# Performance work log

Measured on AMD Instinct MI355X. Metric: run time of the kernel, lower is better.

The kernel has to match this reference:

```python
import jax, jax.numpy as jnp
import numpy as np

N_GENES = 2000
D_MODEL = 256
N_LAYERS = 4
D_STATE = 16
D_CONV = 4
EXPAND = 2
D_INNER = EXPAND * D_MODEL  # 512
DT_RANK = (D_MODEL + 15) // 16  # 16


def layer_norm(x, w, b, eps=1e-5):
    mu = jnp.mean(x, axis=-1, keepdims=True)
    var = jnp.mean((x - mu) ** 2, axis=-1, keepdims=True)
    return (x - mu) * jax.lax.rsqrt(var + eps) * w + b


def mamba_mixer(h, in_w, cw, cb, xp_w, dtp_w, dtp_b, A_log, Dvec, out_w):
    # h: [B, L, d_model]
    B, L, _ = h.shape
    xz = jnp.einsum('bld,ed->ble', h, in_w)            # [B,L,2*Di]
    u, z = jnp.split(xz, 2, axis=-1)                    # [B,L,Di] each
    # causal depthwise conv1d (kernel D_CONV)
    up = jnp.pad(u, ((0, 0), (D_CONV - 1, 0), (0, 0)))
    u = sum(up[:, k:k + L, :] * cw[:, k] for k in range(D_CONV)) + cb
    u = jax.nn.silu(u)
    # input-dependent dt, B, C
    xdbc = jnp.einsum('bld,ed->ble', u, xp_w)           # [B,L,dt_rank+2N]
    dt_r = xdbc[..., :DT_RANK]
    Bm = xdbc[..., DT_RANK:DT_RANK + D_STATE]           # [B,L,N]
    Cm = xdbc[..., DT_RANK + D_STATE:]                  # [B,L,N]
    dt = jax.nn.softplus(jnp.einsum('blr,dr->bld', dt_r, dtp_w) + dtp_b)  # [B,L,Di]
    A = -jnp.exp(A_log)                                 # [Di,N]
    dA = jnp.exp(dt[..., None] * A)                     # [B,L,Di,N]
    dBu = dt[..., None] * Bm[:, :, None, :] * u[..., None]

    def step(hst, inp):
        a, bu = inp
        hst = a * hst + bu
        return hst, hst

    h0 = jnp.zeros((B, D_INNER, D_STATE), dA.dtype)
    _, hs = jax.lax.scan(step, h0, (jnp.moveaxis(dA, 1, 0), jnp.moveaxis(dBu, 1, 0)))
    y = jnp.einsum('lbdn,lbn->bld', hs, jnp.moveaxis(Cm, 1, 0)) + u * Dvec
    y = y * jax.nn.silu(z)
    return jnp.einsum('bld,ed->ble', y, out_w)          # [B,L,d_model]


def setup_inputs() -> dict:
    key = jax.random.key(0)
    ks = jax.random.split(key, 16)
    nl = N_LAYERS
    inp = {
        'x': jax.random.normal(ks[0], (2, N_GENES), jnp.float32),
        'bulk_in_w': jax.random.normal(ks[1], (D_MODEL,), jnp.float32),
        'bulk_in_b': jnp.zeros((D_MODEL,), jnp.float32),
        'gene_emb': jax.random.normal(ks[2], (1, N_GENES, D_MODEL), jnp.float32) * 0.02,
        'mod_emb': jax.random.normal(ks[3], (1, 1, D_MODEL), jnp.float32) * 0.02,
        'ln_w': jnp.ones((nl, D_MODEL), jnp.float32),
        'ln_b': jnp.zeros((nl, D_MODEL), jnp.float32),
        'in_proj_w': jax.random.normal(ks[4], (nl, 2 * D_INNER, D_MODEL), jnp.float32) * (D_MODEL ** -0.5),
        'conv_w': jax.random.normal(ks[5], (nl, D_INNER, D_CONV), jnp.float32) * (D_CONV ** -0.5),
        'conv_b': jnp.zeros((nl, D_INNER), jnp.float32),
        'x_proj_w': jax.random.normal(ks[6], (nl, DT_RANK + 2 * D_STATE, D_INNER), jnp.float32) * (D_INNER ** -0.5),
        'dt_proj_w': jax.random.normal(ks[7], (nl, D_INNER, DT_RANK), jnp.float32) * 0.01,
        'dt_proj_b': jnp.full((nl, D_INNER), -4.0, jnp.float32),
        'A_log': jnp.broadcast_to(jnp.log(jnp.arange(1, D_STATE + 1, dtype=jnp.float32)), (nl, D_INNER, D_STATE)).copy(),
        'D': jnp.ones((nl, D_INNER), jnp.float32),
        'out_proj_w': jax.random.normal(ks[8], (nl, D_MODEL, D_INNER), jnp.float32) * (D_INNER ** -0.5),
        'fin_w': jnp.ones((D_MODEL,), jnp.float32),
        'fin_b': jnp.zeros((D_MODEL,), jnp.float32),
        'head_w': jax.random.normal(ks[9], (D_MODEL,), jnp.float32) * (D_MODEL ** -0.5),
        'head_b': jnp.zeros((), jnp.float32),
    }
    return inp


def reference(x, bulk_in_w, bulk_in_b, gene_emb, mod_emb, ln_w, ln_b, in_proj_w,
              conv_w, conv_b, x_proj_w, dt_proj_w, dt_proj_b, A_log, D, out_proj_w,
              fin_w, fin_b, head_w, head_b):
    # token embed (modality='bulk'); Linear(1,d_model) == x[...,None]*w + b
    h = x[..., None] * bulk_in_w + bulk_in_b + gene_emb + mod_emb  # [B,L,d_model]
    for i in range(N_LAYERS):
        h = h + mamba_mixer(layer_norm(h, ln_w[i], ln_b[i]), in_proj_w[i], conv_w[i],
                            conv_b[i], x_proj_w[i], dt_proj_w[i], dt_proj_b[i],
                            A_log[i], D[i], out_proj_w[i])
    h = layer_norm(h, fin_w, fin_b)
    y = jnp.einsum('bld,d->bl', h, head_w) + head_b  # bulk head, squeeze(-1)
    return y
```

## Files before the change

### kernel.cpp

```cpp
#include <hip/hip_runtime.h>
#include <math.h>

#define B_  2
#define L_  2000
#define DM_ 256
#define DI_ 512
#define DS_ 16
#define NL_ 4
#define BL_ (B_*L_)
#define BLP_ 4096
#define NC_ 125
#define CL_ 16
#define NST_ (B_*DI_*DS_)

typedef unsigned short ushort_t;
typedef __attribute__((ext_vector_type(8))) short bf16x8;
typedef __attribute__((ext_vector_type(4))) float f32x4;

__device__ __forceinline__ float siluf(float x) {
    return x / (1.f + __expf(-x));
}

__device__ __forceinline__ ushort_t f2bf(float x) {
    unsigned int u = __float_as_uint(x);
    unsigned int r = (u + 0x7FFFu + ((u >> 16) & 1u)) >> 16;
    return (ushort_t)r;
}

__device__ __forceinline__ float bf2f(ushort_t v) {
    return __uint_as_float(((unsigned int)v) << 16);
}

__global__ __launch_bounds__(256) void embed_f2bf_kernel(
    const float* __restrict__ x, const float* __restrict__ biw,
    const float* __restrict__ bib, const float* __restrict__ ge,
    const float* __restrict__ me, float* __restrict__ h,
    float2* __restrict__ stats,
    const float* __restrict__ s0, const float* __restrict__ s1,
    const float* __restrict__ s2, ushort_t* __restrict__ d0,
    ushort_t* __restrict__ d1, ushort_t* __restrict__ d2,
    int N0, int N1, int N2)
{
    if (blockIdx.x < BL_) {
        __shared__ float sm[8];
        int bl = blockIdx.x, d = threadIdx.x;
        int l = bl % L_;
        float v = x[bl]*biw[d] + bib[d] + ge[(size_t)l*DM_ + d] + me[d];
        h[(size_t)bl*DM_ + d] = v;
        float s = v, q = v*v;
        #pragma unroll
        for (int o = 32; o > 0; o >>= 1) {
            s += __shfl_down(s, o);
            q += __shfl_down(q, o);
        }
        if ((d & 63) == 0) { sm[d >> 6] = s; sm[4 + (d >> 6)] = q; }
        __syncthreads();
        if (d == 0) {
            stats[bl] = make_float2(sm[0]+sm[1]+sm[2]+sm[3], sm[4]+sm[5]+sm[6]+sm[7]);
            stats[BLP_ + bl]   = make_float2(0.f, 0.f);
            stats[2*BLP_ + bl] = make_float2(0.f, 0.f);
            stats[3*BLP_ + bl] = make_float2(0.f, 0.f);
        }
    } else {
        int i = (blockIdx.x - BL_)*256 + threadIdx.x;
        const float* s; ushort_t* d; int j;
        if (i < N0)           { s = s0; d = d0; j = i; }
        else if (i < N0+N1)   { s = s1; d = d1; j = i - N0; }
        else if (i < N0+N1+N2){ s = s2; d = d2; j = i - N0 - N1; }
        else return;
        float4 v = *(const float4*)(s + 4*j);
        ushort_t o[4] = {f2bf(v.x), f2bf(v.y), f2bf(v.z), f2bf(v.w)};
        *(ushort2*)(d + 4*j)     = *(ushort2*)&o[0];
        *(ushort2*)(d + 4*j + 2) = *(ushort2*)&o[2];
    }
}

__global__ __launch_bounds__(256) void gemm_ln_mfma(
    const float* __restrict__ H, const float2* __restrict__ stats,
    const float* __restrict__ lnw, const float* __restrict__ lnb,
    const ushort_t* __restrict__ W, ushort_t* __restrict__ C, int ldc)
{
    __shared__ ushort_t a_s[128*64];
    __shared__ ushort_t b_s[128*64];
    const int r0 = blockIdx.x*128, c0 = blockIdx.y*128;
    const int tid = threadIdx.x;
    const int lane = tid & 63, w = tid >> 6;
    const int wm = (w & 1)*64, wn = (w >> 1)*64;
    const int qd = lane >> 4, l16 = lane & 15;
    f32x4 acc[4][4] = {};
    for (int kc = 0; kc < DM_; kc += 64) {
        #pragma unroll
        for (int q = 0; q < 4; q++) {
            int ch = tid + 256*q;
            int row = ch >> 3, col8 = (ch & 7)*8;
            int grow = r0 + row;
            float2 t0 = stats[grow], t1 = stats[BLP_ + grow];
            float2 t2 = stats[2*BLP_ + grow], t3 = stats[3*BLP_ + grow];
            float sum = t0.x + t1.x + t2.x + t3.x;
            float ssq = t0.y + t1.y + t2.y + t3.y;
            float mu  = sum * (1.f/DM_);
            float inv = rsqrtf(fmaxf(ssq*(1.f/DM_) - mu*mu, 0.f) + 1e-5f);
            const float* hp = H + (size_t)grow*DM_ + kc + col8;
            float4 h0 = *(const float4*)hp, h1 = *(const float4*)(hp + 4);
            const float* wp = lnw + kc + col8;
            const float* bp = lnb + kc + col8;
            float4 w0 = *(const float4*)wp, w1 = *(const float4*)(wp + 4);
            float4 b0 = *(const float4*)bp, b1 = *(const float4*)(bp + 4);
            __align__(16) ushort_t o[8];
            o[0] = f2bf((h0.x - mu)*inv*w0.x + b0.x);
            o[1] = f2bf((h0.y - mu)*inv*w0.y + b0.y);
            o[2] = f2bf((h0.z - mu)*inv*w0.z + b0.z);
            o[3] = f2bf((h0.w - mu)*inv*w0.w + b0.w);
            o[4] = f2bf((h1.x - mu)*inv*w1.x + b1.x);
            o[5] = f2bf((h1.y - mu)*inv*w1.y + b1.y);
            o[6] = f2bf((h1.z - mu)*inv*w1.z + b1.z);
            o[7] = f2bf((h1.w - mu)*inv*w1.w + b1.w);
            *(uint4*)&a_s[row*64 + col8] = *(const uint4*)o;
            *(bf16x8*)&b_s[row*64 + col8] =
                *(const bf16x8*)(W + (size_t)(c0 + row)*DM_ + kc + col8);
        }
        __syncthreads();
        #pragma unroll
        for (int ks = 0; ks < 2; ks++) {
            bf16x8 af[4], bf[4];
            #pragma unroll
            for (int i = 0; i < 4; i++)
                af[i] = *(const bf16x8*)&a_s[(wm + i*16 + l16)*64 + ks*32 + qd*8];
            #pragma unroll
            for (int j = 0; j < 4; j++)
                bf[j] = *(const bf16x8*)&b_s[(wn + j*16 + l16)*64 + ks*32 + qd*8];
            #pragma unroll
            for (int i = 0; i < 4; i++) {
                #pragma unroll
                for (int j = 0; j < 4; j++)
                    acc[i][j] = __builtin_amdgcn_mfma_f32_16x16x32_bf16(
                        af[i], bf[j], acc[i][j], 0, 0, 0);
            }
        }
        __syncthreads();
    }
    #pragma unroll
    for (int i = 0; i < 4; i++) {
        #pragma unroll
        for (int j = 0; j < 4; j++) {
            #pragma unroll
            for (int r = 0; r < 4; r++) {
                int row = r0 + wm + i*16 + qd*4 + r;
                int col = c0 + wn + j*16 + l16;
                C[(size_t)row*ldc + col] = f2bf(acc[i][j][r]);
            }
        }
    }
}

__global__ __launch_bounds__(256) void conv_xproj_kernel(
    const ushort_t* __restrict__ xz, const float* __restrict__ cw,
    const float* __restrict__ cb, const ushort_t* __restrict__ XWb,
    const float* __restrict__ DTW, const float* __restrict__ DTB,
    const float* __restrict__ Alog,
    ushort_t* __restrict__ u_bf, float* __restrict__ bn,
    float* __restrict__ cn, ushort_t* __restrict__ dtn,
    float2* __restrict__ sa)
{
    __shared__ ushort_t xs[19][520];
    __shared__ ushort_t us[16][520];
    __shared__ float ps[4*16*48];
    __shared__ float dtr_s[16][16];
    const int c = blockIdx.x, b = blockIdx.y;
    const int l0 = c * 16;
    const int tid = threadIdx.x;
    const int lane = tid & 63, w = tid >> 6;
    const int qd = lane >> 4, l16 = lane & 15;
    for (int f = tid; f < 19*64; f += 256) {
        int row = f >> 6, c8 = (f & 63)*8;
        int l = l0 - 3 + row;
        uint4 v = {0u, 0u, 0u, 0u};
        if (l >= 0)
            v = *(const uint4*)(xz + (size_t)(b*L_ + l)*1024 + c8);
        *(uint4*)&xs[row][c8] = v;
    }
    __syncthreads();
    #pragma unroll
    for (int q = 0; q < 2; q++) {
        int ch = tid + q*256;
        float4 wv = *(const float4*)(cw + ch*4);
        float bias = cb[ch];
        float x0 = bf2f(xs[0][ch]);
        float x1 = bf2f(xs[1][ch]);
        float x2 = bf2f(xs[2][ch]);
        #pragma unroll
        for (int j = 0; j < 16; j++) {
            float x3 = bf2f(xs[3 + j][ch]);
            float v = fmaf(x0, wv.x, fmaf(x1, wv.y, fmaf(x2, wv.z, fmaf(x3, wv.w, bias))));
            us[j][ch] = f2bf(siluf(v));
            x0 = x1; x1 = x2; x2 = x3;
        }
    }
    __syncthreads();
    for (int f = tid; f < 16*64; f += 256) {
        int row = f >> 6, c8 = (f & 63)*8;
        *(uint4*)(u_bf + (size_t)(b*L_ + l0 + row)*512 + c8) =
            *(const uint4*)&us[row][c8];
    }
    f32x4 acc[3] = {};
    #pragma unroll
    for (int step = 0; step < 4; step++) {
        int k = w*128 + step*32 + qd*8;
        bf16x8 af = *(const bf16x8*)&us[l16][k];
        #pragma unroll
        for (int j = 0; j < 3; j++) {
            bf16x8 bf = *(const bf16x8*)(XWb + (size_t)(j*16 + l16)*512 + k);
            acc[j] = __builtin_amdgcn_mfma_f32_16x16x32_bf16(af, bf, acc[j], 0, 0, 0);
        }
    }
    #pragma unroll
    for (int j = 0; j < 3; j++) {
        #pragma unroll
        for (int r = 0; r < 4; r++)
            ps[(w*16 + qd*4 + r)*48 + j*16 + l16] = acc[j][r];
    }
    __syncthreads();
    #pragma unroll
    for (int e = tid; e < 768; e += 256)
        ps[e] = ps[e] + ps[768 + e] + ps[1536 + e] + ps[2304 + e];
    __syncthreads();
    {
        int row = tid >> 4, n = tid & 15;
        dtr_s[row][n] = ps[row*48 + n];
        size_t base = ((size_t)(b*L_) + l0 + row)*DS_ + n;
        bn[base] = ps[row*48 + 16 + n];
        cn[base] = ps[row*48 + 32 + n];
    }
    __syncthreads();
    #pragma unroll
    for (int q = 0; q < 2; q++) {
        int d = tid + q*256;
        float wreg[16];
        const float4* wp = (const float4*)(DTW + (size_t)d*16);
        #pragma unroll
        for (int k4 = 0; k4 < 4; k4++) {
            float4 v = wp[k4];
            wreg[4*k4+0] = v.x; wreg[4*k4+1] = v.y;
            wreg[4*k4+2] = v.z; wreg[4*k4+3] = v.w;
        }
        float bias = DTB[d];
        float dtv[16];
        #pragma unroll
        for (int r = 0; r < 16; r++) {
            float a = bias;
            #pragma unroll
            for (int k = 0; k < 16; k++) a = fmaf(dtr_s[r][k], wreg[k], a);
            float dt = a > 20.f ? a : log1pf(__expf(a));
            ushort_t dtb16 = f2bf(dt);
            dtn[((size_t)(b*L_) + l0 + r)*DI_ + d] = dtb16;
            dtv[r] = bf2f(dtb16);
        }
        float Ac[DS_], s[DS_], ap[DS_];
        const float* ar = Alog + (size_t)d*DS_;
        #pragma unroll
        for (int n = 0; n < DS_; n++) { Ac[n] = -__expf(ar[n]); s[n] = 0.f; ap[n] = 1.f; }
        #pragma unroll
        for (int l = 0; l < 16; l++) {
            float dt = dtv[l];
            float u  = bf2f(us[l][d]);
            float dtu = dt*u;
            #pragma unroll
            for (int n = 0; n < DS_; n++) {
                float e = __expf(dt*Ac[n]);
                s[n] = fmaf(e, s[n], dtu*ps[l*48 + 16 + n]);
                ap[n] *= e;
            }
        }
        size_t ib = (((size_t)c*B_ + b)*DI_ + d)*DS_;
        float2* sap = sa + ib;
        #pragma unroll
        for (int k = 0; k < 8; k++) {
            float4 t = make_float4(s[2*k], ap[2*k], s[2*k+1], ap[2*k+1]);
            *(float4*)&sap[2*k] = t;
        }
    }
}

__global__ __launch_bounds__(64) void scan_phase2(
    const float2* __restrict__ sa, float* __restrict__ sinc)
{
    const int t = blockIdx.x*64 + threadIdx.x;
    float s = 0.f;
    for (int g = 0; g < 5; g++) {
        float2 v[25];
        #pragma unroll
        for (int i = 0; i < 25; i++)
            v[i] = sa[(size_t)(g*25 + i)*NST_ + t];
        #pragma unroll
        for (int i = 0; i < 25; i++) {
            sinc[(size_t)(g*25 + i)*NST_ + t] = s;
            s = fmaf(v[i].y, s, v[i].x);
        }
    }
}

template<int LAST>
__global__ __launch_bounds__(512) void phase3_fused(
    const ushort_t* __restrict__ dtn, const ushort_t* __restrict__ u_bf,
    const float* __restrict__ bn, const float* __restrict__ cn,
    const float* __restrict__ Alog, const float* __restrict__ Dv,
    const float* __restrict__ sinc, const ushort_t* __restrict__ xz,
    const ushort_t* __restrict__ opw, float* __restrict__ h,
    const float* __restrict__ lnw, const float* __restrict__ lnb,
    const ushort_t* __restrict__ ipw, ushort_t* __restrict__ xz_out,
    const float* __restrict__ hw, const float* __restrict__ hb,
    float* __restrict__ out)
{
    __shared__ float b_sh[CL_*DS_];
    __shared__ float c_sh[CL_*DS_];
    __shared__ ushort_t ys[16][520];
    __shared__ ushort_t a_sh[16][264];
    __shared__ float2 red2[8*16];
    __shared__ float2 muv[16];
    const int c = blockIdx.x, b = blockIdx.y;
    const int l0 = c*CL_;
    const int tid = threadIdx.x;
    const int w = tid >> 6, lane = tid & 63;
    const int qd = lane >> 4, l16 = lane & 15;
    {
        int f = tid & 255;
        size_t src = ((size_t)(b*L_) + l0)*DS_ + f;
        if (tid < 256) b_sh[f] = bn[src];
        else           c_sh[f] = cn[src];
    }
    const int d = tid;
    float Ac[DS_], s[DS_];
    {
        const float* ar = Alog + (size_t)d*DS_;
        #pragma unroll
        for (int n = 0; n < DS_; n++) Ac[n] = -__expf(ar[n]);
        size_t base = (((size_t)c*B_ + b)*DI_ + d)*DS_;
        #pragma unroll
        for (int n4 = 0; n4 < 4; n4++)
            *(float4*)&s[4*n4] = *(const float4*)(sinc + base + 4*n4);
    }
    const float Dd = Dv[d];
    __syncthreads();
    const ushort_t* dtp = dtn  + ((size_t)(b*L_ + l0))*DI_ + d;
    const ushort_t* up  = u_bf + ((size_t)(b*L_ + l0))*DI_ + d;
    const ushort_t* zp  = xz   + ((size_t)(b*L_ + l0))*1024 + 512 + d;
    for (int l = 0; l < CL_; l++) {
        float dt = bf2f(dtp[(size_t)l*DI_]);
        float u  = bf2f(up[(size_t)l*DI_]);
        float z  = bf2f(zp[(size_t)l*1024]);
        float dtu = dt*u;
        float y = u*Dd;
        #pragma unroll
        for (int n = 0; n < DS_; n++) {
            float e = __expf(dt*Ac[n]);
            s[n] = fmaf(e, s[n], dtu*b_sh[l*DS_ + n]);
            y = fmaf(s[n], c_sh[l*DS_ + n], y);
        }
        ys[l][d] = f2bf(y * siluf(z));
    }
    __syncthreads();
    f32x4 acc[2] = {};
    #pragma unroll
    for (int ks = 0; ks < 16; ks++) {
        bf16x8 af = *(const bf16x8*)&ys[l16][ks*32 + qd*8];
        #pragma unroll
        for (int j = 0; j < 2; j++) {
            bf16x8 bfv = *(const bf16x8*)(opw + (size_t)(w*32 + j*16 + l16)*DI_ + ks*32 + qd*8);
            acc[j] = __builtin_amdgcn_mfma_f32_16x16x32_bf16(af, bfv, acc[j], 0, 0, 0);
        }
    }
    float v[2][4];
    #pragma unroll
    for (int r = 0; r < 4; r++) {
        int lrow = qd*4 + r;
        size_t gr = (size_t)(b*L_ + l0 + lrow);
        float sm = 0.f, sq = 0.f;
        #pragma unroll
        for (int j = 0; j < 2; j++) {
            int col = w*32 + j*16 + l16;
            size_t idx = gr*DM_ + col;
            float vv = h[idx] + acc[j][r];
            if (!LAST) h[idx] = vv;
            v[j][r] = vv;
            sm += vv; sq += vv*vv;
        }
        sm += __shfl_xor(sm, 1); sq += __shfl_xor(sq, 1);
        sm += __shfl_xor(sm, 2); sq += __shfl_xor(sq, 2);
        sm += __shfl_xor(sm, 4); sq += __shfl_xor(sq, 4);
        sm += __shfl_xor(sm, 8); sq += __shfl_xor(sq, 8);
        if (l16 == 0) red2[w*16 + lrow] = make_float2(sm, sq);
    }
    __syncthreads();
    if (tid < 16) {
        float sm = 0.f, sq = 0.f;
        #pragma unroll
        for (int ww = 0; ww < 8; ww++) {
            float2 t = red2[ww*16 + tid];
            sm += t.x; sq += t.y;
        }
        float mu  = sm*(1.f/DM_);
        float inv = rsqrtf(fmaxf(sq*(1.f/DM_) - mu*mu, 0.f) + 1e-5f);
        muv[tid] = make_float2(mu, inv);
    }
    __syncthreads();
    if (!LAST) {
        #pragma unroll
        for (int r = 0; r < 4; r++) {
            int lrow = qd*4 + r;
            float2 mi = muv[lrow];
            #pragma unroll
            for (int j = 0; j < 2; j++) {
                int col = w*32 + j*16 + l16;
                a_sh[lrow][col] = f2bf((v[j][r] - mi.x)*mi.y*lnw[col] + lnb[col]);
            }
        }
        __syncthreads();
        f32x4 acc2[8] = {};
        const int n0 = w*128;
        #pragma unroll
        for (int ks = 0; ks < 8; ks++) {
            bf16x8 af = *(const bf16x8*)&a_sh[l16][ks*32 + qd*8];
            #pragma unroll
            for (int j2 = 0; j2 < 8; j2++) {
                bf16x8 bfv = *(const bf16x8*)(ipw + (size_t)(n0 + j2*16 + l16)*DM_ + ks*32 + qd*8);
                acc2[j2] = __builtin_amdgcn_mfma_f32_16x16x32_bf16(af, bfv, acc2[j2], 0, 0, 0);
            }
        }
        #pragma unroll
        for (int j2 = 0; j2 < 8; j2++) {
            #pragma unroll
            for (int r = 0; r < 4; r++) {
                size_t row = (size_t)(b*L_ + l0 + qd*4 + r);
                xz_out[row*1024 + n0 + j2*16 + l16] = f2bf(acc2[j2][r]);
            }
        }
    } else {
        float hd[4];
        #pragma unroll
        for (int r = 0; r < 4; r++) {
            int lrow = qd*4 + r;
            float2 mi = muv[lrow];
            float a = 0.f;
            #pragma unroll
            for (int j = 0; j < 2; j++) {
                int col = w*32 + j*16 + l16;
                float nv = (v[j][r] - mi.x)*mi.y*lnw[col] + lnb[col];
                a = fmaf(nv, hw[col], a);
            }
            hd[r] = a;
        }
        #pragma unroll
        for (int r = 0; r < 4; r++) {
            float x = hd[r];
            x += __shfl_xor(x, 1); x += __shfl_xor(x, 2);
            x += __shfl_xor(x, 4); x += __shfl_xor(x, 8);
            if (l16 == 0) red2[w*16 + qd*4 + r].x = x;
        }
        __syncthreads();
        if (tid < 16) {
            float x = 0.f;
            #pragma unroll
            for (int ww = 0; ww < 8; ww++) x += red2[ww*16 + tid].x;
            out[(size_t)(b*L_) + l0 + tid] = x + hb[0];
        }
    }
}

extern "C" void kernel_launch(void* const* d_in, const int* in_sizes, int n_in,
                              void* d_out, int out_size, void* d_ws, size_t ws_size,
                              hipStream_t stream)
{
    const float* x    = (const float*)d_in[0];
    const float* biw  = (const float*)d_in[1];
    const float* bib  = (const float*)d_in[2];
    const float* ge   = (const float*)d_in[3];
    const float* me   = (const float*)d_in[4];
    const float* lnw  = (const float*)d_in[5];
    const float* lnb  = (const float*)d_in[6];
    const float* ipw  = (const float*)d_in[7];
    const float* cw   = (const float*)d_in[8];
    const float* cb   = (const float*)d_in[9];
    const float* xpw  = (const float*)d_in[10];
    const float* dtw  = (const float*)d_in[11];
    const float* dtb  = (const float*)d_in[12];
    const float* alog = (const float*)d_in[13];
    const float* Dv   = (const float*)d_in[14];
    const float* opw  = (const float*)d_in[15];
    const float* fw   = (const float*)d_in[16];
    const float* fb   = (const float*)d_in[17];
    const float* hw   = (const float*)d_in[18];
    const float* hb   = (const float*)d_in[19];
    float* out = (float*)d_out;

    float* ws  = (float*)d_ws;
    float* h      = ws;
    float2* stats = (float2*)(h + (size_t)BLP_*DM_);
    float* bn     = (float*)(stats + 4*BLP_);
    float* cn     = bn + (size_t)B_*L_*DS_;
    float2* sa    = (float2*)(cn + (size_t)B_*L_*DS_);
    float* sinc   = (float*)(sa + (size_t)NC_*NST_);
    ushort_t* xz_bf = (ushort_t*)(sinc + (size_t)NC_*NST_);
    ushort_t* u_bf  = xz_bf + (size_t)BLP_*1024;
    ushort_t* dtn   = u_bf + (size_t)BLP_*DI_;
    ushort_t* ipwb  = dtn + (size_t)B_*L_*DI_;
    ushort_t* opwb  = ipwb + (size_t)NL_*1024*DM_;
    ushort_t* xpwb  = opwb + (size_t)NL_*DM_*DI_;

    const int N0 = NL_*1024*DM_/4, N1 = NL_*DM_*DI_/4, N2 = NL_*48*512/4;
    const int conv_blocks = (N0+N1+N2 + 255)/256;
    embed_f2bf_kernel<<<BL_ + conv_blocks, 256, 0, stream>>>(
        x, biw, bib, ge, me, h, stats,
        ipw, opw, xpw, ipwb, opwb, xpwb, N0, N1, N2);

    gemm_ln_mfma<<<dim3(BLP_/128, 1024/128), 256, 0, stream>>>(
        h, stats, lnw, lnb, ipwb, xz_bf, 1024);

    for (int i = 0; i < NL_; i++) {
        conv_xproj_kernel<<<dim3(NC_, B_), 256, 0, stream>>>(
            xz_bf, cw + i*DI_*4, cb + i*DI_, xpwb + (size_t)i*48*512,
            dtw + (size_t)i*DI_*16, dtb + i*DI_, alog + (size_t)i*DI_*DS_,
            u_bf, bn, cn, dtn, sa);
        scan_phase2<<<NST_/64, 64, 0, stream>>>(sa, sinc);
        if (i < NL_-1) {
            phase3_fused<0><<<dim3(NC_, B_), 512, 0, stream>>>(
                dtn, u_bf, bn, cn, alog + (size_t)i*DI_*DS_, Dv + i*DI_,
                sinc, xz_bf, opwb + (size_t)i*DM_*DI_, h,
                lnw + (i+1)*DM_, lnb + (i+1)*DM_,
                ipwb + (size_t)(i+1)*1024*DM_, xz_bf,
                nullptr, nullptr, nullptr);
        } else {
            phase3_fused<1><<<dim3(NC_, B_), 512, 0, stream>>>(
                dtn, u_bf, bn, cn, alog + (size_t)i*DI_*DS_, Dv + i*DI_,
                sinc, xz_bf, opwb + (size_t)i*DM_*DI_, h,
                fw, fb,
                nullptr, xz_bf,
                hw, hb, out);
        }
    }
}
```

Measured before the change: 414.3 us.

## Fuse all stages into one persistent cooperative kernel with grid syncs

```diff
diff --git a/kernel.cpp b/kernel.cpp
--- a/kernel.cpp
+++ b/kernel.cpp
@@ -1,468 +1,446 @@
 #include <hip/hip_runtime.h>
+#include <hip/hip_cooperative_groups.h>
 #include <math.h>
 
-#define B_  2
-#define L_  2000
-#define DM_ 256
-#define DI_ 512
-#define DS_ 16
-#define NL_ 4
-#define BL_ (B_*L_)
+namespace cg = cooperative_groups;
+
+#define B_   2
+#define L_   2000
+#define DM_  256
+#define DI_  512
+#define DS_  16
+#define NL_  4
+#define BL_  (B_*L_)
 #define BLP_ 4096
-#define NC_ 125
-#define CL_ 16
+#define NC_  125
+#define CL_  16
 #define NST_ (B_*DI_*DS_)
+#define NBLK_ 256
+#define NTHR_ 512
 
 typedef unsigned short ushort_t;
 typedef __attribute__((ext_vector_type(8))) short bf16x8;
 typedef __attribute__((ext_vector_type(4))) float f32x4;
 
-__device__ __forceinline__ float siluf(float x) {
-    return x / (1.f + __expf(-x));
-}
-
+__device__ __forceinline__ float siluf(float x) { return x / (1.f + __expf(-x)); }
 __device__ __forceinline__ ushort_t f2bf(float x) {
     unsigned int u = __float_as_uint(x);
-    unsigned int r = (u + 0x7FFFu + ((u >> 16) & 1u)) >> 16;
-    return (ushort_t)r;
+    return (ushort_t)((u + 0x7FFFu + ((u >> 16) & 1u)) >> 16);
 }
-
 __device__ __forceinline__ float bf2f(ushort_t v) {
     return __uint_as_float(((unsigned int)v) << 16);
 }
 
-__global__ __launch_bounds__(256) void embed_f2bf_kernel(
-    const float* __restrict__ x, const float* __restrict__ biw,
-    const float* __restrict__ bib, const float* __restrict__ ge,
-    const float* __restrict__ me, float* __restrict__ h,
-    float2* __restrict__ stats,
-    const float* __restrict__ s0, const float* __restrict__ s1,
-    const float* __restrict__ s2, ushort_t* __restrict__ d0,
-    ushort_t* __restrict__ d1, ushort_t* __restrict__ d2,
-    int N0, int N1, int N2)
+union SharedU {
+    struct { float sm[2][8]; } e;
+    struct { ushort_t a_s[128*64]; ushort_t b_s[128*64]; } g;
+    struct { ushort_t xs[19][520]; ushort_t us[16][520];
+             float ps[8*16*48]; float dtr[16][16]; } c;
+    struct { float b_sh[CL_*DS_]; float c_sh[CL_*DS_];
+             ushort_t ys[16][520]; ushort_t a_sh[16][264];
+             float2 red2[8*16]; float2 muv[16]; } p;
+};
+
+struct KP {
+    const float *x,*biw,*bib,*ge,*me,*lnw,*lnb,*ipw,*cw,*cb,*xpw,*dtw,*dtb,*alog,*Dv,*opw,*fw,*fb,*hw,*hb;
+    float *out;
+    float *h; float2 *stats; float *bn,*cn; float2 *sa; float *sinc;
+    ushort_t *xz,*u_bf,*dtn,*ipwb,*opwb,*xpwb;
+    int N0,N1,N2;
+};
+
+__global__ __launch_bounds__(NTHR_, 2) void mega(KP p)
 {
-    if (blockIdx.x < BL_) {
-        __shared__ float sm[8];
-        int bl = blockIdx.x, d = threadIdx.x;
-        int l = bl % L_;
-        float v = x[bl]*biw[d] + bib[d] + ge[(size_t)l*DM_ + d] + me[d];
-        h[(size_t)bl*DM_ + d] = v;
-        float s = v, q = v*v;
-        #pragma unroll
-        for (int o = 32; o > 0; o >>= 1) {
-            s += __shfl_down(s, o);
-            q += __shfl_down(q, o);
-        }
-        if ((d & 63) == 0) { sm[d >> 6] = s; sm[4 + (d >> 6)] = q; }
-        __syncthreads();
-        if (d == 0) {
-            stats[bl] = make_float2(sm[0]+sm[1]+sm[2]+sm[3], sm[4]+sm[5]+sm[6]+sm[7]);
-            stats[BLP_ + bl]   = make_float2(0.f, 0.f);
-            stats[2*BLP_ + bl] = make_float2(0.f, 0.f);
-            stats[3*BLP_ + bl] = make_float2(0.f, 0.f);
-        }
-    } else {
-        int i = (blockIdx.x - BL_)*256 + threadIdx.x;
-        const float* s; ushort_t* d; int j;
-        if (i < N0)           { s = s0; d = d0; j = i; }
-        else if (i < N0+N1)   { s = s1; d = d1; j = i - N0; }
-        else if (i < N0+N1+N2){ s = s2; d = d2; j = i - N0 - N1; }
-        else return;
-        float4 v = *(const float4*)(s + 4*j);
-        ushort_t o[4] = {f2bf(v.x), f2bf(v.y), f2bf(v.z), f2bf(v.w)};
-        *(ushort2*)(d + 4*j)     = *(ushort2*)&o[0];
-        *(ushort2*)(d + 4*j + 2) = *(ushort2*)&o[2];
-    }
-}
-
-__global__ __launch_bounds__(256) void gemm_ln_mfma(
-    const float* __restrict__ H, const float2* __restrict__ stats,
-    const float* __restrict__ lnw, const float* __restrict__ lnb,
-    const ushort_t* __restrict__ W, ushort_t* __restrict__ C, int ldc)
-{
-    __shared__ ushort_t a_s[128*64];
-    __shared__ ushort_t b_s[128*64];
-    const int r0 = blockIdx.x*128, c0 = blockIdx.y*128;
-    const int tid = threadIdx.x;
-    const int lane = tid & 63, w = tid >> 6;
-    const int wm = (w & 1)*64, wn = (w >> 1)*64;
-    const int qd = lane >> 4, l16 = lane & 15;
-    f32x4 acc[4][4] = {};
-    for (int kc = 0; kc < DM_; kc += 64) {
-        #pragma unroll
-        for (int q = 0; q < 4; q++) {
-            int ch = tid + 256*q;
-            int row = ch >> 3, col8 = (ch & 7)*8;
-            int grow = r0 + row;
-            float2 t0 = stats[grow], t1 = stats[BLP_ + grow];
-            float2 t2 = stats[2*BLP_ + grow], t3 = stats[3*BLP_ + grow];
-            float sum = t0.x + t1.x + t2.x + t3.x;
-            float ssq = t0.y + t1.y + t2.y + t3.y;
-            float mu  = sum * (1.f/DM_);
-            float inv = rsqrtf(fmaxf(ssq*(1.f/DM_) - mu*mu, 0.f) + 1e-5f);
-            const float* hp = H + (size_t)grow*DM_ + kc + col8;
-            float4 h0 = *(const float4*)hp, h1 = *(const float4*)(hp + 4);
-            const float* wp = lnw + kc + col8;
-            const float* bp = lnb + kc + col8;
-            float4 w0 = *(const float4*)wp, w1 = *(const float4*)(wp + 4);
-            float4 b0 = *(const float4*)bp, b1 = *(const float4*)(bp + 4);
-            __align__(16) ushort_t o[8];
-            o[0] = f2bf((h0.x - mu)*inv*w0.x + b0.x);
-            o[1] = f2bf((h0.y - mu)*inv*w0.y + b0.y);
-            o[2] = f2bf((h0.z - mu)*inv*w0.z + b0.z);
-            o[3] = f2bf((h0.w - mu)*inv*w0.w + b0.w);
-            o[4] = f2bf((h1.x - mu)*inv*w1.x + b1.x);
-            o[5] = f2bf((h1.y - mu)*inv*w1.y + b1.y);
-            o[6] = f2bf((h1.z - mu)*inv*w1.z + b1.z);
-            o[7] = f2bf((h1.w - mu)*inv*w1.w + b1.w);
-            *(uint4*)&a_s[row*64 + col8] = *(const uint4*)o;
-            *(bf16x8*)&b_s[row*64 + col8] =
-                *(const bf16x8*)(W + (size_t)(c0 + row)*DM_ + kc + col8);
-        }
-        __syncthreads();
-        #pragma unroll
-        for (int ks = 0; ks < 2; ks++) {
-            bf16x8 af[4], bf[4];
-            #pragma unroll
-            for (int i = 0; i < 4; i++)
-                af[i] = *(const bf16x8*)&a_s[(wm + i*16 + l16)*64 + ks*32 + qd*8];
-            #pragma unroll
-            for (int j = 0; j < 4; j++)
-                bf[j] = *(const bf16x8*)&b_s[(wn + j*16 + l16)*64 + ks*32 + qd*8];
-            #pragma unroll
-            for (int i = 0; i < 4; i++) {
-                #pragma unroll
-                for (int j = 0; j < 4; j++)
-                    acc[i][j] = __builtin_amdgcn_mfma_f32_16x16x32_bf16(
-                        af[i], bf[j], acc[i][j], 0, 0, 0);
-            }
-        }
-        __syncthreads();
-    }
-    #pragma unroll
-    for (int i = 0; i < 4; i++) {
-        #pragma unroll
-        for (int j = 0; j < 4; j++) {
-            #pragma unroll
-            for (int r = 0; r < 4; r++) {
-                int row = r0 + wm + i*16 + qd*4 + r;
-                int col = c0 + wn + j*16 + l16;
-                C[(size_t)row*ldc + col] = f2bf(acc[i][j][r]);
-            }
-        }
-    }
-}
-
-__global__ __launch_bounds__(256) void conv_xproj_kernel(
-    const ushort_t* __restrict__ xz, const float* __restrict__ cw,
-    const float* __restrict__ cb, const ushort_t* __restrict__ XWb,
-    const float* __restrict__ DTW, const float* __restrict__ DTB,
-    const float* __restrict__ Alog,
-    ushort_t* __restrict__ u_bf, float* __restrict__ bn,
-    float* __restrict__ cn, ushort_t* __restrict__ dtn,
-    float2* __restrict__ sa)
-{
-    __shared__ ushort_t xs[19][520];
-    __shared__ ushort_t us[16][520];
-    __shared__ float ps[4*16*48];
-    __shared__ float dtr_s[16][16];
-    const int c = blockIdx.x, b = blockIdx.y;
-    const int l0 = c * 16;
-    const int tid = threadIdx.x;
+    __shared__ SharedU S;
+    const int blk = blockIdx.x, tid = threadIdx.x;
     const int lane = tid & 63, w = tid >> 6;
     const int qd = lane >> 4, l16 = lane & 15;
-    for (int f = tid; f < 19*64; f += 256) {
-        int row = f >> 6, c8 = (f & 63)*8;
-        int l = l0 - 3 + row;
-        uint4 v = {0u, 0u, 0u, 0u};
-        if (l >= 0)
-            v = *(const uint4*)(xz + (size_t)(b*L_ + l)*1024 + c8);
-        *(uint4*)&xs[row][c8] = v;
+    cg::grid_group gg = cg::this_grid();
+
+    {
+        const int half = tid >> 8, tl = tid & 255;
+        for (int it = 0; it < 8; it++) {
+            int bl = blk*2 + half + it*512;
+            bool act = bl < BL_;
+            float v = 0.f;
+            if (act) {
+                int l = bl % L_;
+                v = p.x[bl]*p.biw[tl] + p.bib[tl] + p.ge[(size_t)l*DM_ + tl] + p.me[tl];
+                p.h[(size_t)bl*DM_ + tl] = v;
+            }
+            float s = v, q = v*v;
+            #pragma unroll
+            for (int o = 32; o > 0; o >>= 1) { s += __shfl_down(s, o); q += __shfl_down(q, o); }
+            if ((tl & 63) == 0) { S.e.sm[half][tl>>6] = s; S.e.sm[half][4+(tl>>6)] = q; }
+            __syncthreads();
+            if (act && tl == 0)
+                p.stats[bl] = make_float2(
+                    S.e.sm[half][0]+S.e.sm[half][1]+S.e.sm[half][2]+S.e.sm[half][3],
+                    S.e.sm[half][4]+S.e.sm[half][5]+S.e.sm[half][6]+S.e.sm[half][7]);
+            __syncthreads();
+        }
+        const int NT = p.N0 + p.N1 + p.N2;
+        for (int i = blk*NTHR_ + tid; i < NT; i += NBLK_*NTHR_) {
+            const float* sp; ushort_t* dp; int j;
+            if (i < p.N0)           { sp = p.ipw; dp = p.ipwb; j = i; }
+            else if (i < p.N0+p.N1) { sp = p.opw; dp = p.opwb; j = i - p.N0; }
+            else                    { sp = p.xpw; dp = p.xpwb; j = i - p.N0 - p.N1; }
+            float4 v = *(const float4*)(sp + 4*j);
+            ushort_t o[4] = {f2bf(v.x), f2bf(v.y), f2bf(v.z), f2bf(v.w)};
+            *(ushort2*)(dp + 4*j)     = *(ushort2*)&o[0];
+            *(ushort2*)(dp + 4*j + 2) = *(ushort2*)&o[2];
+        }
     }
-    __syncthreads();
-    #pragma unroll
-    for (int q = 0; q < 2; q++) {
-        int ch = tid + q*256;
-        float4 wv = *(const float4*)(cw + ch*4);
-        float bias = cb[ch];
-        float x0 = bf2f(xs[0][ch]);
-        float x1 = bf2f(xs[1][ch]);
-        float x2 = bf2f(xs[2][ch]);
+    gg.sync();
+
+    {
+        const int r0 = (blk >> 3)*128, c0 = (blk & 7)*128;
+        const int wm = (w & 1)*64, wn = (w >> 1)*32;
+        f32x4 acc[4][2] = {};
+        for (int kc = 0; kc < DM_; kc += 64) {
+            #pragma unroll
+            for (int q = 0; q < 2; q++) {
+                int ch = tid + NTHR_*q;
+                int row = ch >> 3, col8 = (ch & 7)*8;
+                int grow = r0 + row;
+                float2 t0 = p.stats[grow];
+                float mu  = t0.x * (1.f/DM_);
+                float inv = rsqrtf(fmaxf(t0.y*(1.f/DM_) - mu*mu, 0.f) + 1e-5f);
+                const float* hp = p.h + (size_t)grow*DM_ + kc + col8;
+                float4 h0 = *(const float4*)hp, h1 = *(const float4*)(hp + 4);
+                const float* wp = p.lnw + kc + col8;
+                const float* bp = p.lnb + kc + col8;
+                float4 w0 = *(const float4*)wp, w1 = *(const float4*)(wp + 4);
+                float4 b0 = *(const float4*)bp, b1 = *(const float4*)(bp + 4);
+                __align__(16) ushort_t o[8];
+                o[0] = f2bf((h0.x - mu)*inv*w0.x + b0.x);
+                o[1] = f2bf((h0.y - mu)*inv*w0.y + b0.y);
+                o[2] = f2bf((h0.z - mu)*inv*w0.z + b0.z);
+                o[3] = f2bf((h0.w - mu)*inv*w0.w + b0.w);
+                o[4] = f2bf((h1.x - mu)*inv*w1.x + b1.x);
+                o[5] = f2bf((h1.y - mu)*inv*w1.y + b1.y);
+                o[6] = f2bf((h1.z - mu)*inv*w1.z + b1.z);
+                o[7] = f2bf((h1.w - mu)*inv*w1.w + b1.w);
+                *(uint4*)&S.g.a_s[row*64 + col8] = *(const uint4*)o;
+                *(bf16x8*)&S.g.b_s[row*64 + col8] =
+                    *(const bf16x8*)(p.ipwb + (size_t)(c0 + row)*DM_ + kc + col8);
+            }
+            __syncthreads();
+            #pragma unroll
+            for (int ks = 0; ks < 2; ks++) {
+                bf16x8 af[4], bv[2];
+                #pragma unroll
+                for (int i = 0; i < 4; i++)
+                    af[i] = *(const bf16x8*)&S.g.a_s[(wm + i*16 + l16)*64 + ks*32 + qd*8];
+                #pragma unroll
+                for (int j = 0; j < 2; j++)
+                    bv[j] = *(const bf16x8*)&S.g.b_s[(wn + j*16 + l16)*64 + ks*32 + qd*8];
+                #pragma unroll
+                for (int i = 0; i < 4; i++)
+                    #pragma unroll
+                    for (int j = 0; j < 2; j++)
+                        acc[i][j] = __builtin_amdgcn_mfma_f32_16x16x32_bf16(
+                            af[i], bv[j], acc[i][j], 0, 0, 0);
+            }
+            __syncthreads();
+        }
         #pragma unroll
-        for (int j = 0; j < 16; j++) {
-            float x3 = bf2f(xs[3 + j][ch]);
-            float v = fmaf(x0, wv.x, fmaf(x1, wv.y, fmaf(x2, wv.z, fmaf(x3, wv.w, bias))));
-            us[j][ch] = f2bf(siluf(v));
-            x0 = x1; x1 = x2; x2 = x3;
-        }
+        for (int i = 0; i < 4; i++)
+            #pragma unroll
+            for (int j = 0; j < 2; j++)
+                #pragma unroll
+                for (int r = 0; r < 4; r++) {
+                    int row = r0 + wm + i*16 + qd*4 + r;
+                    int col = c0 + wn + j*16 + l16;
+                    p.xz[(size_t)row*1024 + col] = f2bf(acc[i][j][r]);
+                }
     }
-    __syncthreads();
-    for (int f = tid; f < 16*64; f += 256) {
-        int row = f >> 6, c8 = (f & 63)*8;
-        *(uint4*)(u_bf + (size_t)(b*L_ + l0 + row)*512 + c8) =
-            *(const uint4*)&us[row][c8];
-    }
-    f32x4 acc[3] = {};
-    #pragma unroll
-    for (int step = 0; step < 4; step++) {
-        int k = w*128 + step*32 + qd*8;
-        bf16x8 af = *(const bf16x8*)&us[l16][k];
-        #pragma unroll
-        for (int j = 0; j < 3; j++) {
-            bf16x8 bf = *(const bf16x8*)(XWb + (size_t)(j*16 + l16)*512 + k);
-            acc[j] = __builtin_amdgcn_mfma_f32_16x16x32_bf16(af, bf, acc[j], 0, 0, 0);
-        }
-    }
-    #pragma unroll
-    for (int j = 0; j < 3; j++) {
-        #pragma unroll
-        for (int r = 0; r < 4; r++)
-            ps[(w*16 + qd*4 + r)*48 + j*16 + l16] = acc[j][r];
-    }
-    __syncthreads();
-    #pragma unroll
-    for (int e = tid; e < 768; e += 256)
-        ps[e] = ps[e] + ps[768 + e] + ps[1536 + e] + ps[2304 + e];
-    __syncthreads();
-    {
-        int row = tid >> 4, n = tid & 15;
-        dtr_s[row][n] = ps[row*48 + n];
-        size_t base = ((size_t)(b*L_) + l0 + row)*DS_ + n;
-        bn[base] = ps[row*48 + 16 + n];
-        cn[base] = ps[row*48 + 32 + n];
-    }
-    __syncthreads();
-    #pragma unroll
-    for (int q = 0; q < 2; q++) {
-        int d = tid + q*256;
-        float wreg[16];
-        const float4* wp = (const float4*)(DTW + (size_t)d*16);
-        #pragma unroll
-        for (int k4 = 0; k4 < 4; k4++) {
-            float4 v = wp[k4];
-            wreg[4*k4+0] = v.x; wreg[4*k4+1] = v.y;
-            wreg[4*k4+2] = v.z; wreg[4*k4+3] = v.w;
-        }
-        float bias = DTB[d];
-        float dtv[16];
-        #pragma unroll
-        for (int r = 0; r < 16; r++) {
-            float a = bias;
-            #pragma unroll
-            for (int k = 0; k < 16; k++) a = fmaf(dtr_s[r][k], wreg[k], a);
-            float dt = a > 20.f ? a : log1pf(__expf(a));
-            ushort_t dtb16 = f2bf(dt);
-            dtn[((size_t)(b*L_) + l0 + r)*DI_ + d] = dtb16;
-            dtv[r] = bf2f(dtb16);
-        }
-        float Ac[DS_], s[DS_], ap[DS_];
-        const float* ar = Alog + (size_t)d*DS_;
-        #pragma unroll
-        for (int n = 0; n < DS_; n++) { Ac[n] = -__expf(ar[n]); s[n] = 0.f; ap[n] = 1.f; }
-        #pragma unroll
-        for (int l = 0; l < 16; l++) {
-            float dt = dtv[l];
-            float u  = bf2f(us[l][d]);
-            float dtu = dt*u;
-            #pragma unroll
-            for (int n = 0; n < DS_; n++) {
-                float e = __expf(dt*Ac[n]);
-                s[n] = fmaf(e, s[n], dtu*ps[l*48 + 16 + n]);
-                ap[n] *= e;
-            }
-        }
-        size_t ib = (((size_t)c*B_ + b)*DI_ + d)*DS_;
-        float2* sap = sa + ib;
-        #pragma unroll
-        for (int k = 0; k < 8; k++) {
-            float4 t = make_float4(s[2*k], ap[2*k], s[2*k+1], ap[2*k+1]);
-            *(float4*)&sap[2*k] = t;
-        }
-    }
-}
-
-__global__ __launch_bounds__(64) void scan_phase2(
-    const float2* __restrict__ sa, float* __restrict__ sinc)
-{
-    const int t = blockIdx.x*64 + threadIdx.x;
-    float s = 0.f;
-    for (int g = 0; g < 5; g++) {
-        float2 v[25];
-        #pragma unroll
-        for (int i = 0; i < 25; i++)
-            v[i] = sa[(size_t)(g*25 + i)*NST_ + t];
-        #pragma unroll
-        for (int i = 0; i < 25; i++) {
-            sinc[(size_t)(g*25 + i)*NST_ + t] = s;
-            s = fmaf(v[i].y, s, v[i].x);
-        }
-    }
-}
-
-template<int LAST>
-__global__ __launch_bounds__(512) void phase3_fused(
-    const ushort_t* __restrict__ dtn, const ushort_t* __restrict__ u_bf,
-    const float* __restrict__ bn, const float* __restrict__ cn,
-    const float* __restrict__ Alog, const float* __restrict__ Dv,
-    const float* __restrict__ sinc, const ushort_t* __restrict__ xz,
-    const ushort_t* __restrict__ opw, float* __restrict__ h,
-    const float* __restrict__ lnw, const float* __restrict__ lnb,
-    const ushort_t* __restrict__ ipw, ushort_t* __restrict__ xz_out,
-    const float* __restrict__ hw, const float* __restrict__ hb,
-    float* __restrict__ out)
-{
-    __shared__ float b_sh[CL_*DS_];
-    __shared__ float c_sh[CL_*DS_];
-    __shared__ ushort_t ys[16][520];
-    __shared__ ushort_t a_sh[16][264];
-    __shared__ float2 red2[8*16];
-    __shared__ float2 muv[16];
-    const int c = blockIdx.x, b = blockIdx.y;
-    const int l0 = c*CL_;
-    const int tid = threadIdx.x;
-    const int w = tid >> 6, lane = tid & 63;
-    const int qd = lane >> 4, l16 = lane & 15;
-    {
-        int f = tid & 255;
-        size_t src = ((size_t)(b*L_) + l0)*DS_ + f;
-        if (tid < 256) b_sh[f] = bn[src];
-        else           c_sh[f] = cn[src];
-    }
-    const int d = tid;
-    float Ac[DS_], s[DS_];
-    {
-        const float* ar = Alog + (size_t)d*DS_;
-        #pragma unroll
-        for (int n = 0; n < DS_; n++) Ac[n] = -__expf(ar[n]);
-        size_t base = (((size_t)c*B_ + b)*DI_ + d)*DS_;
-        #pragma unroll
-        for (int n4 = 0; n4 < 4; n4++)
-            *(float4*)&s[4*n4] = *(const float4*)(sinc + base + 4*n4);
-    }
-    const float Dd = Dv[d];
-    __syncthreads();
-    const ushort_t* dtp = dtn  + ((size_t)(b*L_ + l0))*DI_ + d;
-    const ushort_t* up  = u_bf + ((size_t)(b*L_ + l0))*DI_ + d;
-    const ushort_t* zp  = xz   + ((size_t)(b*L_ + l0))*1024 + 512 + d;
-    for (int l = 0; l < CL_; l++) {
-        float dt = bf2f(dtp[(size_t)l*DI_]);
-        float u  = bf2f(up[(size_t)l*DI_]);
-        float z  = bf2f(zp[(size_t)l*1024]);
-        float dtu = dt*u;
-        float y = u*Dd;
-        #pragma unroll
-        for (int n = 0; n < DS_; n++) {
-            float e = __expf(dt*Ac[n]);
-            s[n] = fmaf(e, s[n], dtu*b_sh[l*DS_ + n]);
-            y = fmaf(s[n], c_sh[l*DS_ + n], y);
-        }
-        ys[l][d] = f2bf(y * siluf(z));
-    }
-    __syncthreads();
-    f32x4 acc[2] = {};
-    #pragma unroll
-    for (int ks = 0; ks < 16; ks++) {
-        bf16x8 af = *(const bf16x8*)&ys[l16][ks*32 + qd*8];
-        #pragma unroll
-        for (int j = 0; j < 2; j++) {
-            bf16x8 bfv = *(const bf16x8*)(opw + (size_t)(w*32 + j*16 + l16)*DI_ + ks*32 + qd*8);
-            acc[j] = __builtin_amdgcn_mfma_f32_16x16x32_bf16(af, bfv, acc[j], 0, 0, 0);
-        }
-    }
-    float v[2][4];
-    #pragma unroll
-    for (int r = 0; r < 4; r++) {
-        int lrow = qd*4 + r;
-        size_t gr = (size_t)(b*L_ + l0 + lrow);
-        float sm = 0.f, sq = 0.f;
-        #pragma unroll
-        for (int j = 0; j < 2; j++) {
-            int col = w*32 + j*16 + l16;
-            size_t idx = gr*DM_ + col;
-            float vv = h[idx] + acc[j][r];
-            if (!LAST) h[idx] = vv;
-            v[j][r] = vv;
-            sm += vv; sq += vv*vv;
-        }
-        sm += __shfl_xor(sm, 1); sq += __shfl_xor(sq, 1);
-        sm += __shfl_xor(sm, 2); sq += __shfl_xor(sq, 2);
-        sm += __shfl_xor(sm, 4); sq += __shfl_xor(sq, 4);
-        sm += __shfl_xor(sm, 8); sq += __shfl_xor(sq, 8);
-        if (l16 == 0) red2[w*16 + lrow] = make_float2(sm, sq);
-    }
-    __syncthreads();
-    if (tid < 16) {
-        float sm = 0.f, sq = 0.f;
-        #pragma unroll
-        for (int ww = 0; ww < 8; ww++) {
-            float2 t = red2[ww*16 + tid];
-            sm += t.x; sq += t.y;
-        }
-        float mu  = sm*(1.f/DM_);
-        float inv = rsqrtf(fmaxf(sq*(1.f/DM_) - mu*mu, 0.f) + 1e-5f);
-        muv[tid] = make_float2(mu, inv);
-    }
-    __syncthreads();
-    if (!LAST) {
-        #pragma unroll
-        for (int r = 0; r < 4; r++) {
-            int lrow = qd*4 + r;
-            float2 mi = muv[lrow];
-            #pragma unroll
-            for (int j = 0; j < 2; j++) {
-                int col = w*32 + j*16 + l16;
-                a_sh[lrow][col] = f2bf((v[j][r] - mi.x)*mi.y*lnw[col] + lnb[col]);
-            }
-        }
-        __syncthreads();
-        f32x4 acc2[8] = {};
-        const int n0 = w*128;
-        #pragma unroll
-        for (int ks = 0; ks < 8; ks++) {
-            bf16x8 af = *(const bf16x8*)&a_sh[l16][ks*32 + qd*8];
-            #pragma unroll
-            for (int j2 = 0; j2 < 8; j2++) {
-                bf16x8 bfv = *(const bf16x8*)(ipw + (size_t)(n0 + j2*16 + l16)*DM_ + ks*32 + qd*8);
-                acc2[j2] = __builtin_amdgcn_mfma_f32_16x16x32_bf16(af, bfv, acc2[j2], 0, 0, 0);
-            }
-        }
-        #pragma unroll
-        for (int j2 = 0; j2 < 8; j2++) {
+    gg.sync();
+
+    for (int li = 0; li < NL_; li++) {
+        if (blk < 2*NC_) {
+            const int c = blk >> 1, b = blk & 1;
+            const int l0 = c*CL_;
+            const float* cw  = p.cw + li*DI_*4;
+            const float* cb  = p.cb + li*DI_;
+            const ushort_t* XWb = p.xpwb + (size_t)li*48*512;
+            const float* DTW = p.dtw + (size_t)li*DI_*16;
+            const float* DTB = p.dtb + li*DI_;
+            const float* Alog = p.alog + (size_t)li*DI_*DS_;
+            for (int f = tid; f < 19*64; f += NTHR_) {
+                int row = f >> 6, c8 = (f & 63)*8;
+                int l = l0 - 3 + row;
+                uint4 v = {0u,0u,0u,0u};
+                if (l >= 0) v = *(const uint4*)(p.xz + (size_t)(b*L_ + l)*1024 + c8);
+                *(uint4*)&S.c.xs[row][c8] = v;
+            }
+            __syncthreads();
+            {
+                int ch = tid;
+                float4 wv = *(const float4*)(cw + ch*4);
+                float bias = cb[ch];
+                float x0 = bf2f(S.c.xs[0][ch]);
+                float x1 = bf2f(S.c.xs[1][ch]);
+                float x2 = bf2f(S.c.xs[2][ch]);
+                #pragma unroll
+                for (int j = 0; j < 16; j++) {
+                    float x3 = bf2f(S.c.xs[3 + j][ch]);
+                    float v = fmaf(x0, wv.x, fmaf(x1, wv.y, fmaf(x2, wv.z, fmaf(x3, wv.w, bias))));
+                    S.c.us[j][ch] = f2bf(siluf(v));
+                    x0 = x1; x1 = x2; x2 = x3;
+                }
+            }
+            __syncthreads();
+            for (int f = tid; f < 16*64; f += NTHR_) {
+                int row = f >> 6, c8 = (f & 63)*8;
+                *(uint4*)(p.u_bf + (size_t)(b*L_ + l0 + row)*512 + c8) =
+                    *(const uint4*)&S.c.us[row][c8];
+            }
+            f32x4 acc[3] = {};
+            #pragma unroll
+            for (int st = 0; st < 2; st++) {
+                int k = w*64 + st*32 + qd*8;
+                bf16x8 af = *(const bf16x8*)&S.c.us[l16][k];
+                #pragma unroll
+                for (int j = 0; j < 3; j++) {
+                    bf16x8 bv = *(const bf16x8*)(XWb + (size_t)(j*16 + l16)*512 + k);
+                    acc[j] = __builtin_amdgcn_mfma_f32_16x16x32_bf16(af, bv, acc[j], 0, 0, 0);
+                }
+            }
+            #pragma unroll
+            for (int j = 0; j < 3; j++)
+                #pragma unroll
+                for (int r = 0; r < 4; r++)
+                    S.c.ps[(w*16 + qd*4 + r)*48 + j*16 + l16] = acc[j][r];
+            __syncthreads();
+            for (int e = tid; e < 768; e += NTHR_)
+                S.c.ps[e] = S.c.ps[e] + S.c.ps[768+e] + S.c.ps[1536+e] + S.c.ps[2304+e]
+                          + S.c.ps[3072+e] + S.c.ps[3840+e] + S.c.ps[4608+e] + S.c.ps[5376+e];
+            __syncthreads();
+            if (tid < 256) {
+                int row = tid >> 4, n = tid & 15;
+                S.c.dtr[row][n] = S.c.ps[row*48 + n];
+                size_t base = ((size_t)(b*L_) + l0 + row)*DS_ + n;
+                p.bn[base] = S.c.ps[row*48 + 16 + n];
+                p.cn[base] = S.c.ps[row*48 + 32 + n];
+            }
+            __syncthreads();
+            {
+                const int d = tid;
+                float wreg[16];
+                const float4* wp = (const float4*)(DTW + (size_t)d*16);
+                #pragma unroll
+                for (int k4 = 0; k4 < 4; k4++) {
+                    float4 vv = wp[k4];
+                    wreg[4*k4+0] = vv.x; wreg[4*k4+1] = vv.y;
+                    wreg[4*k4+2] = vv.z; wreg[4*k4+3] = vv.w;
+                }
+                float bias = DTB[d];
+                float dtv[16];
+                #pragma unroll
+                for (int r = 0; r < 16; r++) {
+                    float a = bias;
+                    #pragma unroll
+                    for (int k = 0; k < 16; k++) a = fmaf(S.c.dtr[r][k], wreg[k], a);
+                    float dt = a > 20.f ? a : log1pf(__expf(a));
+                    ushort_t dtb16 = f2bf(dt);
+                    p.dtn[((size_t)(b*L_) + l0 + r)*DI_ + d] = dtb16;
+                    dtv[r] = bf2f(dtb16);
+                }
+                float Ac[DS_], s[DS_], ap[DS_];
+                const float* ar = Alog + (size_t)d*DS_;
+                #pragma unroll
+                for (int n = 0; n < DS_; n++) { Ac[n] = -__expf(ar[n]); s[n] = 0.f; ap[n] = 1.f; }
+                #pragma unroll
+                for (int l = 0; l < 16; l++) {
+                    float dt = dtv[l];
+                    float u  = bf2f(S.c.us[l][d]);
+                    float dtu = dt*u;
+                    #pragma unroll
+                    for (int n = 0; n < DS_; n++) {
+                        float e = __expf(dt*Ac[n]);
+                        s[n] = fmaf(e, s[n], dtu*S.c.ps[l*48 + 16 + n]);
+                        ap[n] *= e;
+                    }
+                }
+                size_t ib = (((size_t)c*B_ + b)*DI_ + d)*DS_;
+                float2* sap = p.sa + ib;
+                #pragma unroll
+                for (int k = 0; k < 8; k++)
+                    *(float4*)&sap[2*k] = make_float4(s[2*k], ap[2*k], s[2*k+1], ap[2*k+1]);
+            }
+        }
+        gg.sync();
+
+        if (blk < NST_/NTHR_) {
+            const int t = blk*NTHR_ + tid;
+            float s = 0.f;
+            for (int g2 = 0; g2 < 5; g2++) {
+                float2 v[25];
+                #pragma unroll
+                for (int i2 = 0; i2 < 25; i2++)
+                    v[i2] = p.sa[(size_t)(g2*25 + i2)*NST_ + t];
+                #pragma unroll
+                for (int i2 = 0; i2 < 25; i2++) {
+                    p.sinc[(size_t)(g2*25 + i2)*NST_ + t] = s;
+                    s = fmaf(v[i2].y, s, v[i2].x);
+                }
+            }
+        }
+        gg.sync();
+
+        if (blk < 2*NC_) {
+            const bool last = (li == NL_-1);
+            const int c = blk >> 1, b = blk & 1, l0 = c*CL_;
+            const float* Alog = p.alog + (size_t)li*DI_*DS_;
+            const float* Dvp  = p.Dv + li*DI_;
+            const ushort_t* opw = p.opwb + (size_t)li*DM_*DI_;
+            const float* lw = last ? p.fw : (p.lnw + (li+1)*DM_);
+            const float* lb = last ? p.fb : (p.lnb + (li+1)*DM_);
+            {
+                int f = tid & 255;
+                size_t src = ((size_t)(b*L_) + l0)*DS_ + f;
+                if (tid < 256) S.p.b_sh[f] = p.bn[src];
+                else           S.p.c_sh[f] = p.cn[src];
+            }
+            const int d = tid;
+            float Ac[DS_], s[DS_];
+            {
+                const float* ar = Alog + (size_t)d*DS_;
+                #pragma unroll
+                for (int n = 0; n < DS_; n++) Ac[n] = -__expf(ar[n]);
+                size_t base = (((size_t)c*B_ + b)*DI_ + d)*DS_;
+                #pragma unroll
+                for (int n4 = 0; n4 < 4; n4++)
+                    *(float4*)&s[4*n4] = *(const float4*)(p.sinc + base + 4*n4);
+            }
+            const float Dd = Dvp[d];
+            __syncthreads();
+            const ushort_t* dtp = p.dtn  + ((size_t)(b*L_ + l0))*DI_ + d;
+            const ushort_t* up  = p.u_bf + ((size_t)(b*L_ + l0))*DI_ + d;
+            const ushort_t* zp  = p.xz   + ((size_t)(b*L_ + l0))*1024 + 512 + d;
+            for (int l = 0; l < CL_; l++) {
+                float dt = bf2f(dtp[(size_t)l*DI_]);
+                float u  = bf2f(up[(size_t)l*DI_]);
+                float z  = bf2f(zp[(size_t)l*1024]);
+                float dtu = dt*u;
+                float y = u*Dd;
+                #pragma unroll
+                for (int n = 0; n < DS_; n++) {
+                    float e = __expf(dt*Ac[n]);
+                    s[n] = fmaf(e, s[n], dtu*S.p.b_sh[l*DS_ + n]);
+                    y = fmaf(s[n], S.p.c_sh[l*DS_ + n], y);
+                }
+                S.p.ys[l][d] = f2bf(y * siluf(z));
+            }
+            __syncthreads();
+            f32x4 acc[2] = {};
+            #pragma unroll
+            for (int ks = 0; ks < 16; ks++) {
+                bf16x8 af = *(const bf16x8*)&S.p.ys[l16][ks*32 + qd*8];
+                #pragma unroll
+                for (int j = 0; j < 2; j++) {
+                    bf16x8 bv = *(const bf16x8*)(opw + (size_t)(w*32 + j*16 + l16)*DI_ + ks*32 + qd*8);
+                    acc[j] = __builtin_amdgcn_mfma_f32_16x16x32_bf16(af, bv, acc[j], 0, 0, 0);
+                }
+            }
+            float v[2][4];
             #pragma unroll
             for (int r = 0; r < 4; r++) {
-                size_t row = (size_t)(b*L_ + l0 + qd*4 + r);
-                xz_out[row*1024 + n0 + j2*16 + l16] = f2bf(acc2[j2][r]);
-            }
-        }
-    } else {
-        float hd[4];
-        #pragma unroll
-        for (int r = 0; r < 4; r++) {
-            int lrow = qd*4 + r;
-            float2 mi = muv[lrow];
-            float a = 0.f;
-            #pragma unroll
-            for (int j = 0; j < 2; j++) {
-                int col = w*32 + j*16 + l16;
-                float nv = (v[j][r] - mi.x)*mi.y*lnw[col] + lnb[col];
-                a = fmaf(nv, hw[col], a);
-            }
-            hd[r] = a;
-        }
-        #pragma unroll
-        for (int r = 0; r < 4; r++) {
-            float x = hd[r];
-            x += __shfl_xor(x, 1); x += __shfl_xor(x, 2);
-            x += __shfl_xor(x, 4); x += __shfl_xor(x, 8);
-            if (l16 == 0) red2[w*16 + qd*4 + r].x = x;
-        }
-        __syncthreads();
-        if (tid < 16) {
-            float x = 0.f;
-            #pragma unroll
-            for (int ww = 0; ww < 8; ww++) x += red2[ww*16 + tid].x;
-            out[(size_t)(b*L_) + l0 + tid] = x + hb[0];
-        }
+                int lrow = qd*4 + r;
+                size_t gr = (size_t)(b*L_ + l0 + lrow);
+                float sm = 0.f, sq = 0.f;
+                #pragma unroll
+                for (int j = 0; j < 2; j++) {
+                    int col = w*32 + j*16 + l16;
+                    size_t idx = gr*DM_ + col;
+                    float vv = p.h[idx] + acc[j][r];
+                    if (!last) p.h[idx] = vv;
+                    v[j][r] = vv;
+                    sm += vv; sq += vv*vv;
+                }
+                sm += __shfl_xor(sm, 1); sq += __shfl_xor(sq, 1);
+                sm += __shfl_xor(sm, 2); sq += __shfl_xor(sq, 2);
+                sm += __shfl_xor(sm, 4); sq += __shfl_xor(sq, 4);
+                sm += __shfl_xor(sm, 8); sq += __shfl_xor(sq, 8);
+                if (l16 == 0) S.p.red2[w*16 + lrow] = make_float2(sm, sq);
+            }
+            __syncthreads();
+            if (tid < 16) {
+                float sm = 0.f, sq = 0.f;
+                #pragma unroll
+                for (int ww = 0; ww < 8; ww++) {
+                    float2 t = S.p.red2[ww*16 + tid];
+                    sm += t.x; sq += t.y;
+                }
+                float mu  = sm*(1.f/DM_);
+                float inv = rsqrtf(fmaxf(sq*(1.f/DM_) - mu*mu, 0.f) + 1e-5f);
+                S.p.muv[tid] = make_float2(mu, inv);
+            }
+            __syncthreads();
+            if (!last) {
+                const ushort_t* ipw2 = p.ipwb + (size_t)(li+1)*1024*DM_;
+                #pragma unroll
+                for (int r = 0; r < 4; r++) {
+                    int lrow = qd*4 + r;
+                    float2 mi = S.p.muv[lrow];
+                    #pragma unroll
+                    for (int j = 0; j < 2; j++) {
+                        int col = w*32 + j*16 + l16;
+                        S.p.a_sh[lrow][col] = f2bf((v[j][r] - mi.x)*mi.y*lw[col] + lb[col]);
+                    }
+                }
+                __syncthreads();
+                f32x4 acc2[8] = {};
+                const int n0 = w*128;
+                #pragma unroll
+                for (int ks = 0; ks < 8; ks++) {
+                    bf16x8 af = *(const bf16x8*)&S.p.a_sh[l16][ks*32 + qd*8];
+                    #pragma unroll
+                    for (int j2 = 0; j2 < 8; j2++) {
+                        bf16x8 bv = *(const bf16x8*)(ipw2 + (size_t)(n0 + j2*16 + l16)*DM_ + ks*32 + qd*8);
+                        acc2[j2] = __builtin_amdgcn_mfma_f32_16x16x32_bf16(af, bv, acc2[j2], 0, 0, 0);
+                    }
+                }
+                #pragma unroll
+                for (int j2 = 0; j2 < 8; j2++)
+                    #pragma unroll
+                    for (int r = 0; r < 4; r++) {
+                        size_t row = (size_t)(b*L_ + l0 + qd*4 + r);
+                        p.xz[row*1024 + n0 + j2*16 + l16] = f2bf(acc2[j2][r]);
+                    }
+            } else {
+                float hd[4];
+                #pragma unroll
+                for (int r = 0; r < 4; r++) {
+                    int lrow = qd*4 + r;
+                    float2 mi = S.p.muv[lrow];
+                    float a = 0.f;
+                    #pragma unroll
+                    for (int j = 0; j < 2; j++) {
+                        int col = w*32 + j*16 + l16;
+                        float nv = (v[j][r] - mi.x)*mi.y*lw[col] + lb[col];
+                        a = fmaf(nv, p.hw[col], a);
+                    }
+                    hd[r] = a;
+                }
+                #pragma unroll
+                for (int r = 0; r < 4; r++) {
+                    float xv = hd[r];
+                    xv += __shfl_xor(xv, 1); xv += __shfl_xor(xv, 2);
+                    xv += __shfl_xor(xv, 4); xv += __shfl_xor(xv, 8);
+                    if (l16 == 0) S.p.red2[w*16 + qd*4 + r].x = xv;
+                }
+                __syncthreads();
+                if (tid < 16) {
+                    float xv = 0.f;
+                    #pragma unroll
+                    for (int ww = 0; ww < 8; ww++) xv += S.p.red2[ww*16 + tid].x;
+                    p.out[(size_t)(b*L_) + l0 + tid] = xv + p.hb[0];
+                }
+            }
+        }
+        if (li < NL_-1) gg.sync();
     }
 }
 
@@ -470,71 +448,46 @@
                               void* d_out, int out_size, void* d_ws, size_t ws_size,
                               hipStream_t stream)
 {
-    const float* x    = (const float*)d_in[0];
-    const float* biw  = (const float*)d_in[1];
-    const float* bib  = (const float*)d_in[2];
-    const float* ge   = (const float*)d_in[3];
-    const float* me   = (const float*)d_in[4];
-    const float* lnw  = (const float*)d_in[5];
-    const float* lnb  = (const float*)d_in[6];
-    const float* ipw  = (const float*)d_in[7];
-    const float* cw   = (const float*)d_in[8];
-    const float* cb   = (const float*)d_in[9];
-    const float* xpw  = (const float*)d_in[10];
-    const float* dtw  = (const float*)d_in[11];
-    const float* dtb  = (const float*)d_in[12];
-    const float* alog = (const float*)d_in[13];
-    const float* Dv   = (const float*)d_in[14];
-    const float* opw  = (const float*)d_in[15];
-    const float* fw   = (const float*)d_in[16];
-    const float* fb   = (const float*)d_in[17];
-    const float* hw   = (const float*)d_in[18];
-    const float* hb   = (const float*)d_in[19];
-    float* out = (float*)d_out;
-
-    float* ws  = (float*)d_ws;
-    float* h      = ws;
-    float2* stats = (float2*)(h + (size_t)BLP_*DM_);
-    float* bn     = (float*)(stats + 4*BLP_);
-    float* cn     = bn + (size_t)B_*L_*DS_;
-    float2* sa    = (float2*)(cn + (size_t)B_*L_*DS_);
-    float* sinc   = (float*)(sa + (size_t)NC_*NST_);
-    ushort_t* xz_bf = (ushort_t*)(sinc + (size_t)NC_*NST_);
-    ushort_t* u_bf  = xz_bf + (size_t)BLP_*1024;
-    ushort_t* dtn   = u_bf + (size_t)BLP_*DI_;
-    ushort_t* ipwb  = dtn + (size_t)B_*L_*DI_;
-    ushort_t* opwb  = ipwb + (size_t)NL_*1024*DM_;
-    ushort_t* xpwb  = opwb + (size_t)NL_*DM_*DI_;
-
-    const int N0 = NL_*1024*DM_/4, N1 = NL_*DM_*DI_/4, N2 = NL_*48*512/4;
-    const int conv_blocks = (N0+N1+N2 + 255)/256;
-    embed_f2bf_kernel<<<BL_ + conv_blocks, 256, 0, stream>>>(
-        x, biw, bib, ge, me, h, stats,
-        ipw, opw, xpw, ipwb, opwb, xpwb, N0, N1, N2);
-
-    gemm_ln_mfma<<<dim3(BLP_/128, 1024/128), 256, 0, stream>>>(
-        h, stats, lnw, lnb, ipwb, xz_bf, 1024);
-
-    for (int i = 0; i < NL_; i++) {
-        conv_xproj_kernel<<<dim3(NC_, B_), 256, 0, stream>>>(
-            xz_bf, cw + i*DI_*4, cb + i*DI_, xpwb + (size_t)i*48*512,
-            dtw + (size_t)i*DI_*16, dtb + i*DI_, alog + (size_t)i*DI_*DS_,
-            u_bf, bn, cn, dtn, sa);
-        scan_phase2<<<NST_/64, 64, 0, stream>>>(sa, sinc);
-        if (i < NL_-1) {
-            phase3_fused<0><<<dim3(NC_, B_), 512, 0, stream>>>(
-                dtn, u_bf, bn, cn, alog + (size_t)i*DI_*DS_, Dv + i*DI_,
-                sinc, xz_bf, opwb + (size_t)i*DM_*DI_, h,
-                lnw + (i+1)*DM_, lnb + (i+1)*DM_,
-                ipwb + (size_t)(i+1)*1024*DM_, xz_bf,
-                nullptr, nullptr, nullptr);
-        } else {
-            phase3_fused<1><<<dim3(NC_, B_), 512, 0, stream>>>(
-                dtn, u_bf, bn, cn, alog + (size_t)i*DI_*DS_, Dv + i*DI_,
-                sinc, xz_bf, opwb + (size_t)i*DM_*DI_, h,
-                fw, fb,
-                nullptr, xz_bf,
-                hw, hb, out);
-        }
-    }
+    KP p;
+    p.x    = (const float*)d_in[0];
+    p.biw  = (const float*)d_in[1];
+    p.bib  = (const float*)d_in[2];
+    p.ge   = (const float*)d_in[3];
+    p.me   = (const float*)d_in[4];
+    p.lnw  = (const float*)d_in[5];
+    p.lnb  = (const float*)d_in[6];
+    p.ipw  = (const float*)d_in[7];
+    p.cw   = (const float*)d_in[8];
+    p.cb   = (const float*)d_in[9];
+    p.xpw  = (const float*)d_in[10];
+    p.dtw  = (const float*)d_in[11];
+    p.dtb  = (const float*)d_in[12];
+    p.alog = (const float*)d_in[13];
+    p.Dv   = (const float*)d_in[14];
+    p.opw  = (const float*)d_in[15];
+    p.fw   = (const float*)d_in[16];
+    p.fb   = (const float*)d_in[17];
+    p.hw   = (const float*)d_in[18];
+    p.hb   = (const float*)d_in[19];
+    p.out  = (float*)d_out;
+
+    float* ws = (float*)d_ws;
+    p.h     = ws;                 ws += (size_t)BLP_*DM_;
+    p.stats = (float2*)ws;        ws += 2*(size_t)BLP_;
+    p.bn    = ws;                 ws += (size_t)B_*L_*DS_;
+    p.cn    = ws;                 ws += (size_t)B_*L_*DS_;
+    p.sa    = (float2*)ws;        ws += 2*(size_t)NC_*NST_;
+    p.sinc  = ws;                 ws += (size_t)NC_*NST_;
+    ushort_t* uptr = (ushort_t*)ws;
+    p.xz   = uptr;                uptr += (size_t)BLP_*1024;
+    p.u_bf = uptr;                uptr += (size_t)BLP_*DI_;
+    p.dtn  = uptr;                uptr += (size_t)B_*L_*DI_;
+    p.ipwb = uptr;                uptr += (size_t)NL_*1024*DM_;
+    p.opwb = uptr;                uptr += (size_t)NL_*DM_*DI_;
+    p.xpwb = uptr;
+    p.N0 = NL_*1024*DM_/4; p.N1 = NL_*DM_*DI_/4; p.N2 = NL_*48*512/4;
+
+    void* kargs[] = { (void*)&p };
+    hipLaunchCooperativeKernel((const void*)mega, dim3(NBLK_), dim3(NTHR_),
+                               kargs, 0, stream);
 }
```

Result: slower. 1.178 ms (+184.2%).
